# Optimization experiments

Measured on AMD Instinct MI355X. Metric: run time of the kernel, lower is better.

Reference implementation:

```python
import jax, jax.numpy as jnp
import numpy as np

B, N, DIM = 8, 16384, 256
DIM_HEAD, NUM_HEADS = 64, 8
D = DIM_HEAD * NUM_HEADS  # 512
SCALE = DIM_HEAD ** (-0.5)


def setup_inputs() -> dict:
    key = jax.random.key(0)
    ks = jax.random.split(key, 11)
    s = 0.02
    return {
        "x": jax.random.normal(ks[0], (B, N, DIM), dtype=jnp.float32),
        "Wq": jax.random.normal(ks[1], (DIM, D), dtype=jnp.float32) * s,
        "bq": jax.random.normal(ks[2], (D,), dtype=jnp.float32) * s,
        "Wk": jax.random.normal(ks[3], (DIM, D), dtype=jnp.float32) * s,
        "bk": jax.random.normal(ks[4], (D,), dtype=jnp.float32) * s,
        "qw": jax.random.normal(ks[5], (D, 1), dtype=jnp.float32),  # query_weight parameter
        "Wp": jax.random.normal(ks[6], (D, D), dtype=jnp.float32) * s,
        "bp": jax.random.normal(ks[7], (D,), dtype=jnp.float32) * s,
        "Wo": jax.random.normal(ks[8], (D, DIM_HEAD), dtype=jnp.float32) * s,
        "bo": jax.random.normal(ks[9], (DIM_HEAD,), dtype=jnp.float32) * s,
    }


def reference(x, Wq, bq, Wk, bk, qw, Wp, bp, Wo, bo):
    # query, key: [B, N, D]
    query = jnp.einsum("bnc,cd->bnd", x, Wq) + bq
    key = jnp.einsum("bnc,cd->bnd", x, Wk) + bk
    # per-token scalar score: [B, N, 1]
    score = (query @ qw) * SCALE
    # global attention context: sum over sequence axis -> [B, 1, D]
    attn_weight = jnp.sum(score * query, axis=1, keepdims=True)
    # broadcast (repeat over N), gate keys, project, residual add of query
    out = jnp.einsum("bnd,de->bne", attn_weight * key, Wp) + bp + query
    # output projection D -> dim_head: [B, N, DIM_HEAD]
    out = jnp.einsum("bnd,dh->bnh", out, Wo) + bo
    return out
```

## Files before the change

### kernel.cpp

```cpp
#include <hip/hip_runtime.h>
#include <hip/hip_bf16.h>


#define NN 16384
#define CC 256
#define DD 512
#define HH 64
#define SCALE_F 0.125f

#define OFF_SX    0
#define OFF_TSUM  2048
#define OFF_WQQ   2056
#define OFF_BQQ   2312
#define OFF_WPWO  2320
#define OFF_WQWO  35088
#define OFF_CBIAS 51472
#define OFF_BEFF  51536
#define OFF_WEFFT 52048

typedef unsigned short ushort_t;
typedef __attribute__((ext_vector_type(8))) short short8;
typedef __attribute__((ext_vector_type(4))) float floatx4;

__device__ __forceinline__ unsigned short f2bf(float f) {
    __hip_bfloat16 h = __float2bfloat16(f);
    return __builtin_bit_cast(unsigned short, h);
}

__global__ __launch_bounds__(256) void k_prep(
    const float* __restrict__ Wq, const float* __restrict__ bq,
    const float* __restrict__ qw, const float* __restrict__ Wp,
    const float* __restrict__ bp, const float* __restrict__ Wo,
    const float* __restrict__ bo, float* __restrict__ ws)
{
    __shared__ float lds[2056];
    const int tid = threadIdx.x;
    const int bid = blockIdx.x;

    if (bid < 128) {
        const int d0 = bid * 4;
        for (int i = tid; i < 2048; i += 256) lds[i] = Wp[d0 * 512 + i];
        __syncthreads();
        const int dl = tid >> 6, h = tid & 63;
        float acc = 0.f;
        for (int e = 0; e < 512; ++e)
            acc = fmaf(lds[dl * 512 + e], Wo[e * 64 + h], acc);
        ws[OFF_WPWO + (d0 + dl) * 64 + h] = acc;
    } else if (bid < 192) {
        const int c0 = (bid - 128) * 4;
        for (int i = tid; i < 2048; i += 256) lds[i] = Wq[c0 * 512 + i];
        __syncthreads();
        const int cl = tid >> 6, h = tid & 63;
        float acc = 0.f;
        for (int e = 0; e < 512; ++e)
            acc = fmaf(lds[cl * 512 + e], Wo[e * 64 + h], acc);
        ws[OFF_WQWO + (c0 + cl) * 64 + h] = acc;
    } else if (bid == 192) {
        float* lb = lds + 2048;
        for (int i = tid; i < 512; i += 256) lds[i] = qw[i];
        if (tid == 0) *lb = 0.f;
        __syncthreads();
        const float* wr = Wq + tid * 512;
        float acc = 0.f;
        for (int d = 0; d < 512; ++d) acc = fmaf(wr[d], lds[d], acc);
        ws[OFF_WQQ + tid] = acc;
        float pb = fmaf(bq[tid], lds[tid], bq[tid + 256] * lds[tid + 256]);
#pragma unroll
        for (int m = 1; m < 64; m <<= 1) pb += __shfl_xor(pb, m);
        if ((tid & 63) == 0) atomicAdd(lb, pb);
        __syncthreads();
        if (tid == 0) ws[OFF_BQQ] = *lb;
    } else if (bid == 193) {
        const int h = tid & 63, part = tid >> 6;
        float acc = 0.f;
        for (int d = part * 128; d < part * 128 + 128; ++d)
            acc = fmaf(bq[d] + bp[d], Wo[d * 64 + h], acc);
        lds[part * 64 + h] = acc;
        __syncthreads();
        if (tid < 64)
            ws[OFF_CBIAS + tid] = bo[tid] + lds[tid] + lds[64 + tid] +
                                  lds[128 + tid] + lds[192 + tid];
    } else {
        for (int i = tid; i < 2056; i += 256) ws[OFF_SX + i] = 0.f;
    }
}

__global__ __launch_bounds__(256) void k_phase1(
    const float* __restrict__ x, float* __restrict__ ws)
{
    const int tid  = threadIdx.x;
    const int lane = tid & 63;
    const int wave = tid >> 6;
    const int quad = lane >> 4;
    const int l15  = lane & 15;
    __shared__ float lacc[256];
    __shared__ float ltsum;

    floatx4 wv[4];
#pragma unroll
    for (int j = 0; j < 4; ++j)
        wv[j] = *(const floatx4*)(ws + OFF_WQQ + j * 64 + l15 * 4);
    const float bqq = ws[OFF_BQQ];

    const int vb = blockIdx.x;
    const int b = vb >> 7;
    const int rbase = (vb & 127) * 128;
    lacc[tid] = 0.f;
    if (tid == 0) ltsum = 0.f;
    __syncthreads();

    const float* xb = x + (size_t)b * NN * CC;
    const int r0 = rbase + wave * 32 + quad;
    floatx4 accs[4];
#pragma unroll
    for (int j = 0; j < 4; ++j)
#pragma unroll
        for (int k = 0; k < 4; ++k) accs[j][k] = 0.f;
    float ts = 0.f;

#pragma unroll 2
    for (int it = 0; it < 8; ++it) {
        const float* xr = xb + (size_t)(r0 + it * 4) * CC + l15 * 4;
        const floatx4 x0 = *(const floatx4*)(xr);
        const floatx4 x1 = *(const floatx4*)(xr + 64);
        const floatx4 x2 = *(const floatx4*)(xr + 128);
        const floatx4 x3 = *(const floatx4*)(xr + 192);
        float p = 0.f;
#pragma unroll
        for (int k = 0; k < 4; ++k) {
            p = fmaf(x0[k], wv[0][k], p);
            p = fmaf(x1[k], wv[1][k], p);
            p = fmaf(x2[k], wv[2][k], p);
            p = fmaf(x3[k], wv[3][k], p);
        }
        p += __shfl_xor(p, 1);
        p += __shfl_xor(p, 2);
        p += __shfl_xor(p, 4);
        p += __shfl_xor(p, 8);
        const float t = SCALE_F * (p + bqq);
        ts += t;
#pragma unroll
        for (int k = 0; k < 4; ++k) {
            accs[0][k] = fmaf(t, x0[k], accs[0][k]);
            accs[1][k] = fmaf(t, x1[k], accs[1][k]);
            accs[2][k] = fmaf(t, x2[k], accs[2][k]);
            accs[3][k] = fmaf(t, x3[k], accs[3][k]);
        }
    }

#pragma unroll
    for (int j = 0; j < 4; ++j)
#pragma unroll
        for (int k = 0; k < 4; ++k) {
            float v = accs[j][k];
            v += __shfl_xor(v, 16);
            v += __shfl_xor(v, 32);
            if (quad == 0) atomicAdd(&lacc[j * 64 + l15 * 4 + k], v);
        }
    if (l15 == 0) atomicAdd(&ltsum, ts);
    __syncthreads();
    atomicAdd(&ws[OFF_SX + b * 256 + tid], lacc[tid]);
    if (tid == 0) atomicAdd(&ws[OFF_TSUM + b], ltsum);
}

__global__ __launch_bounds__(256) void k_weff(
    const float* __restrict__ Wq, const float* __restrict__ bq,
    const float* __restrict__ Wk, const float* __restrict__ bk,
    float* __restrict__ ws)
{
    const int tid = threadIdx.x;
    const int b = blockIdx.y;
    const int c0 = blockIdx.x * 4;
    __shared__ float lsx[256];
    __shared__ float law[512];
    __shared__ float lred[256];
    __shared__ float lts;

    lsx[tid] = ws[OFF_SX + b * 256 + tid];
    if (tid == 0) lts = ws[OFF_TSUM + b];
    __syncthreads();
    const float tsum = lts;

    for (int d = tid; d < 512; d += 256) {
        float a0 = 0.f, a1 = 0.f, a2 = 0.f, a3 = 0.f;
        for (int c = 0; c < 256; c += 4) {
            a0 = fmaf(lsx[c + 0], Wq[(c + 0) * 512 + d], a0);
            a1 = fmaf(lsx[c + 1], Wq[(c + 1) * 512 + d], a1);
            a2 = fmaf(lsx[c + 2], Wq[(c + 2) * 512 + d], a2);
            a3 = fmaf(lsx[c + 3], Wq[(c + 3) * 512 + d], a3);
        }
        law[d] = tsum * bq[d] + ((a0 + a1) + (a2 + a3));
    }
    __syncthreads();

    const int cl = tid >> 6, h = tid & 63;
    const int c = c0 + cl;
    const float* wkr = Wk + (size_t)c * 512;
    const float* wp  = ws + OFF_WPWO;
    float a0 = 0.f, a1 = 0.f, a2 = 0.f, a3 = 0.f;
    for (int d = 0; d < 512; d += 4) {
        a0 = fmaf(wkr[d + 0] * law[d + 0], wp[(d + 0) * 64 + h], a0);
        a1 = fmaf(wkr[d + 1] * law[d + 1], wp[(d + 1) * 64 + h], a1);
        a2 = fmaf(wkr[d + 2] * law[d + 2], wp[(d + 2) * 64 + h], a2);
        a3 = fmaf(wkr[d + 3] * law[d + 3], wp[(d + 3) * 64 + h], a3);
    }
    const float acc = ws[OFF_WQWO + c * 64 + h] + ((a0 + a1) + (a2 + a3));

    ushort_t* wt = (ushort_t*)(ws + OFF_WEFFT) + (size_t)b * (HH * CC);
    wt[(size_t)h * CC + c] = f2bf(acc);

    if (blockIdx.x == 0) {
        const int part = tid >> 6;
        float a = 0.f;
        for (int d = part * 128; d < part * 128 + 128; ++d)
            a = fmaf(bk[d] * law[d], wp[d * 64 + h], a);
        lred[tid] = a;
        __syncthreads();
        if (tid < 64)
            ws[OFF_BEFF + b * 64 + tid] = ws[OFF_CBIAS + tid] + lred[tid] +
                lred[64 + tid] + lred[128 + tid] + lred[192 + tid];
    }
}

__global__ __launch_bounds__(256) void k_out(
    const float* __restrict__ x, const float* __restrict__ ws,
    float* __restrict__ out)
{
    const int tid  = threadIdx.x;
    const int lane = tid & 63;
    const int wave = tid >> 6;
    const int quad = lane >> 4;
    const int l15  = lane & 15;
    __shared__ __align__(16) ushort_t lwt[64 * 264];

    const int vb = blockIdx.x;
    const int b = vb >> 7;
    const int rt0 = vb & 127;
    const ushort_t* wt = (const ushort_t*)(ws + OFF_WEFFT) + (size_t)b * (HH * CC);
    for (int o = tid; o < 2048; o += 256) {
        const int h = o >> 5, seg = o & 31;
        *(short8*)(lwt + h * 264 + seg * 8) = *(const short8*)(wt + h * 256 + seg * 8);
    }
    __syncthreads();

    const float* beff = ws + OFF_BEFF + b * 64;
    float bias[4];
#pragma unroll
    for (int ht = 0; ht < 4; ++ht) bias[ht] = beff[ht * 16 + l15];

#pragma unroll
    for (int s = 0; s < 2; ++s) {
        const int row0 = (rt0 + s * 128) * 64 + wave * 16;
        const float* xr = x + ((size_t)b * NN + row0 + l15) * CC + quad * 8;
        short8 afrag[8];
#pragma unroll
        for (int kk = 0; kk < 8; ++kk) {
            const floatx4 u0 = *(const floatx4*)(xr + kk * 32);
            const floatx4 u1 = *(const floatx4*)(xr + kk * 32 + 4);
            short8 t;
            t[0] = (short)f2bf(u0[0]); t[1] = (short)f2bf(u0[1]);
            t[2] = (short)f2bf(u0[2]); t[3] = (short)f2bf(u0[3]);
            t[4] = (short)f2bf(u1[0]); t[5] = (short)f2bf(u1[1]);
            t[6] = (short)f2bf(u1[2]); t[7] = (short)f2bf(u1[3]);
            afrag[kk] = t;
        }
        floatx4 acc[4];
#pragma unroll
        for (int ht = 0; ht < 4; ++ht)
#pragma unroll
            for (int r = 0; r < 4; ++r) acc[ht][r] = 0.f;

#pragma unroll
        for (int kk = 0; kk < 8; ++kk)
#pragma unroll
            for (int ht = 0; ht < 4; ++ht) {
                const short8 bf =
                    *(const short8*)(lwt + (ht * 16 + l15) * 264 + quad * 8 + kk * 32);
                acc[ht] = __builtin_amdgcn_mfma_f32_16x16x32_bf16(
                    afrag[kk], bf, acc[ht], 0, 0, 0);
            }

#pragma unroll
        for (int ht = 0; ht < 4; ++ht) {
            const int h = ht * 16 + l15;
#pragma unroll
            for (int r = 0; r < 4; ++r) {
                const int row = row0 + quad * 4 + r;
                out[((size_t)b * NN + row) * HH + h] = acc[ht][r] + bias[ht];
            }
        }
    }
}

extern "C" void kernel_launch(void* const* d_in, const int* in_sizes, int n_in,
                              void* d_out, int out_size, void* d_ws, size_t ws_size,
                              hipStream_t stream) {
    const float* x  = (const float*)d_in[0];
    const float* Wq = (const float*)d_in[1];
    const float* bq = (const float*)d_in[2];
    const float* Wk = (const float*)d_in[3];
    const float* bk = (const float*)d_in[4];
    const float* qw = (const float*)d_in[5];
    const float* Wp = (const float*)d_in[6];
    const float* bp = (const float*)d_in[7];
    const float* Wo = (const float*)d_in[8];
    const float* bo = (const float*)d_in[9];
    float* ws  = (float*)d_ws;
    float* out = (float*)d_out;

    hipLaunchKernelGGL(k_prep,   dim3(195),    dim3(256), 0, stream,
                       Wq, bq, qw, Wp, bp, Wo, bo, ws);
    hipLaunchKernelGGL(k_phase1, dim3(1024),   dim3(256), 0, stream, x, ws);
    hipLaunchKernelGGL(k_weff,   dim3(64, 8),  dim3(256), 0, stream,
                       Wq, bq, Wk, bk, ws);
    hipLaunchKernelGGL(k_out,    dim3(1024),   dim3(256), 0, stream, x, ws, out);
}
```

Baseline: 308.2 us.

## Hoist attention-weight vector into its own kernel and prefetch x before LDS staging

The Wq·sx reduction that produces the per-batch attention weight vector is moved out of k_weff, where each of 64 blocks per batch recomputed it, into a new small k_aw kernel that writes it once to workspace. k_weff now reads it from global memory. Separately, k_out loads and converts its first x tile before staging the weight matrix into LDS, so the global loads overlap the LDS fill. This adds one kernel launch and a workspace round trip, and the prefetch raises register pressure.

Measured after the change: 301.3 us. 1.02x faster.

```diff
diff --git a/kernel.cpp b/kernel.cpp
--- a/kernel.cpp
+++ b/kernel.cpp
@@ -17,6 +17,7 @@
 #define OFF_CBIAS 51472
 #define OFF_BEFF  51536
 #define OFF_WEFFT 52048
+#define OFF_AW    117584
 
 typedef unsigned short ushort_t;
 typedef __attribute__((ext_vector_type(8))) short short8;
@@ -163,40 +164,47 @@
     if (tid == 0) atomicAdd(&ws[OFF_TSUM + b], ltsum);
 }
 
+__global__ __launch_bounds__(256) void k_aw(
+    const float* __restrict__ Wq, const float* __restrict__ bq,
+    float* __restrict__ ws)
+{
+    const int tid = threadIdx.x;
+    const int b = blockIdx.y;
+    const int d = blockIdx.x * 256 + tid;
+    __shared__ float lsx[256];
+    __shared__ float lts;
+    lsx[tid] = ws[OFF_SX + b * 256 + tid];
+    if (tid == 0) lts = ws[OFF_TSUM + b];
+    __syncthreads();
+
+    float a[8];
+#pragma unroll
+    for (int j = 0; j < 8; ++j) a[j] = 0.f;
+    for (int c = 0; c < 256; c += 8) {
+#pragma unroll
+        for (int j = 0; j < 8; ++j)
+            a[j] = fmaf(lsx[c + j], Wq[(c + j) * 512 + d], a[j]);
+    }
+    const float s = ((a[0] + a[1]) + (a[2] + a[3])) +
+                    ((a[4] + a[5]) + (a[6] + a[7]));
+    ws[OFF_AW + b * 512 + d] = lts * bq[d] + s;
+}
+
 __global__ __launch_bounds__(256) void k_weff(
-    const float* __restrict__ Wq, const float* __restrict__ bq,
     const float* __restrict__ Wk, const float* __restrict__ bk,
     float* __restrict__ ws)
 {
     const int tid = threadIdx.x;
     const int b = blockIdx.y;
     const int c0 = blockIdx.x * 4;
-    __shared__ float lsx[256];
-    __shared__ float law[512];
     __shared__ float lred[256];
-    __shared__ float lts;
-
-    lsx[tid] = ws[OFF_SX + b * 256 + tid];
-    if (tid == 0) lts = ws[OFF_TSUM + b];
-    __syncthreads();
-    const float tsum = lts;
-
-    for (int d = tid; d < 512; d += 256) {
-        float a0 = 0.f, a1 = 0.f, a2 = 0.f, a3 = 0.f;
-        for (int c = 0; c < 256; c += 4) {
-            a0 = fmaf(lsx[c + 0], Wq[(c + 0) * 512 + d], a0);
-            a1 = fmaf(lsx[c + 1], Wq[(c + 1) * 512 + d], a1);
-            a2 = fmaf(lsx[c + 2], Wq[(c + 2) * 512 + d], a2);
-            a3 = fmaf(lsx[c + 3], Wq[(c + 3) * 512 + d], a3);
-        }
-        law[d] = tsum * bq[d] + ((a0 + a1) + (a2 + a3));
-    }
-    __syncthreads();
 
     const int cl = tid >> 6, h = tid & 63;
     const int c = c0 + cl;
+    const float* law = ws + OFF_AW + (size_t)b * 512;
     const float* wkr = Wk + (size_t)c * 512;
     const float* wp  = ws + OFF_WPWO;
+
     float a0 = 0.f, a1 = 0.f, a2 = 0.f, a3 = 0.f;
     for (int d = 0; d < 512; d += 4) {
         a0 = fmaf(wkr[d + 0] * law[d + 0], wp[(d + 0) * 64 + h], a0);
@@ -236,6 +244,22 @@
     const int vb = blockIdx.x;
     const int b = vb >> 7;
     const int rt0 = vb & 127;
+
+    const int row0_0 = rt0 * 64 + wave * 16;
+    const float* xr0 = x + ((size_t)b * NN + row0_0 + l15) * CC + quad * 8;
+    short8 afrag0[8];
+#pragma unroll
+    for (int kk = 0; kk < 8; ++kk) {
+        const floatx4 u0 = *(const floatx4*)(xr0 + kk * 32);
+        const floatx4 u1 = *(const floatx4*)(xr0 + kk * 32 + 4);
+        short8 t;
+        t[0] = (short)f2bf(u0[0]); t[1] = (short)f2bf(u0[1]);
+        t[2] = (short)f2bf(u0[2]); t[3] = (short)f2bf(u0[3]);
+        t[4] = (short)f2bf(u1[0]); t[5] = (short)f2bf(u1[1]);
+        t[6] = (short)f2bf(u1[2]); t[7] = (short)f2bf(u1[3]);
+        afrag0[kk] = t;
+    }
+
     const ushort_t* wt = (const ushort_t*)(ws + OFF_WEFFT) + (size_t)b * (HH * CC);
     for (int o = tid; o < 2048; o += 256) {
         const int h = o >> 5, seg = o & 31;
@@ -248,28 +272,52 @@
 #pragma unroll
     for (int ht = 0; ht < 4; ++ht) bias[ht] = beff[ht * 16 + l15];
 
-#pragma unroll
-    for (int s = 0; s < 2; ++s) {
-        const int row0 = (rt0 + s * 128) * 64 + wave * 16;
-        const float* xr = x + ((size_t)b * NN + row0 + l15) * CC + quad * 8;
-        short8 afrag[8];
+    {
+        floatx4 acc[4];
+#pragma unroll
+        for (int ht = 0; ht < 4; ++ht)
+#pragma unroll
+            for (int r = 0; r < 4; ++r) acc[ht][r] = 0.f;
+#pragma unroll
+        for (int kk = 0; kk < 8; ++kk)
+#pragma unroll
+            for (int ht = 0; ht < 4; ++ht) {
+                const short8 bf =
+                    *(const short8*)(lwt + (ht * 16 + l15) * 264 + quad * 8 + kk * 32);
+                acc[ht] = __builtin_amdgcn_mfma_f32_16x16x32_bf16(
+                    afrag0[kk], bf, acc[ht], 0, 0, 0);
+            }
+#pragma unroll
+        for (int ht = 0; ht < 4; ++ht) {
+            const int h = ht * 16 + l15;
+#pragma unroll
+            for (int r = 0; r < 4; ++r) {
+                const int row = row0_0 + quad * 4 + r;
+                out[((size_t)b * NN + row) * HH + h] = acc[ht][r] + bias[ht];
+            }
+        }
+    }
+
+    {
+        const int row0_1 = (rt0 + 128) * 64 + wave * 16;
+        const float* xr1 = x + ((size_t)b * NN + row0_1 + l15) * CC + quad * 8;
+        short8 afrag1[8];
 #pragma unroll
         for (int kk = 0; kk < 8; ++kk) {
-            const floatx4 u0 = *(const floatx4*)(xr + kk * 32);
-            const floatx4 u1 = *(const floatx4*)(xr + kk * 32 + 4);
+            const floatx4 u0 = *(const floatx4*)(xr1 + kk * 32);
+            const floatx4 u1 = *(const floatx4*)(xr1 + kk * 32 + 4);
             short8 t;
             t[0] = (short)f2bf(u0[0]); t[1] = (short)f2bf(u0[1]);
             t[2] = (short)f2bf(u0[2]); t[3] = (short)f2bf(u0[3]);
             t[4] = (short)f2bf(u1[0]); t[5] = (short)f2bf(u1[1]);
             t[6] = (short)f2bf(u1[2]); t[7] = (short)f2bf(u1[3]);
-            afrag[kk] = t;
+            afrag1[kk] = t;
         }
         floatx4 acc[4];
 #pragma unroll
         for (int ht = 0; ht < 4; ++ht)
 #pragma unroll
             for (int r = 0; r < 4; ++r) acc[ht][r] = 0.f;
-
 #pragma unroll
         for (int kk = 0; kk < 8; ++kk)
 #pragma unroll
@@ -277,15 +325,14 @@
                 const short8 bf =
                     *(const short8*)(lwt + (ht * 16 + l15) * 264 + quad * 8 + kk * 32);
                 acc[ht] = __builtin_amdgcn_mfma_f32_16x16x32_bf16(
-                    afrag[kk], bf, acc[ht], 0, 0, 0);
+                    afrag1[kk], bf, acc[ht], 0, 0, 0);
             }
-
 #pragma unroll
         for (int ht = 0; ht < 4; ++ht) {
             const int h = ht * 16 + l15;
 #pragma unroll
             for (int r = 0; r < 4; ++r) {
-                const int row = row0 + quad * 4 + r;
+                const int row = row0_1 + quad * 4 + r;
                 out[((size_t)b * NN + row) * HH + h] = acc[ht][r] + bias[ht];
             }
         }
@@ -311,7 +358,7 @@
     hipLaunchKernelGGL(k_prep,   dim3(195),    dim3(256), 0, stream,
                        Wq, bq, qw, Wp, bp, Wo, bo, ws);
     hipLaunchKernelGGL(k_phase1, dim3(1024),   dim3(256), 0, stream, x, ws);
-    hipLaunchKernelGGL(k_weff,   dim3(64, 8),  dim3(256), 0, stream,
-                       Wq, bq, Wk, bk, ws);
+    hipLaunchKernelGGL(k_aw,     dim3(2, 8),   dim3(256), 0, stream, Wq, bq, ws);
+    hipLaunchKernelGGL(k_weff,   dim3(64, 8),  dim3(256), 0, stream, Wk, bk, ws);
     hipLaunchKernelGGL(k_out,    dim3(1024),   dim3(256), 0, stream, x, ws, out);
 }
```

## Split attention-weight matvec into its own kernel and reparallelize effective-weight build

Applied to the files above, without the earlier changes.

Adds a separate k_aw kernel that computes the per-batch attention-weight vector once and stores it in the workspace. Before, each of the 64 k_weff blocks per batch recomputed that full 256x512 matvec. k_weff now launches one block per input channel: 16 lane groups each own 4 outputs, the d dimension is split across 16 parts with float4 loads from the fused Wp·Wo matrix, and an LDS tree reduction combines the parts. Both new kernels are launched twice in a row; the second launches are redundant and only add launch and execution overhead.

After: 310.6 us. Within noise of the previous version (+0.8%).

```diff
diff --git a/kernel.cpp b/kernel.cpp
--- a/kernel.cpp
+++ b/kernel.cpp
@@ -17,6 +17,7 @@
 #define OFF_CBIAS 51472
 #define OFF_BEFF  51536
 #define OFF_WEFFT 52048
+#define OFF_AW    117584
 
 typedef unsigned short ushort_t;
 typedef __attribute__((ext_vector_type(8))) short short8;
@@ -163,62 +164,105 @@
     if (tid == 0) atomicAdd(&ws[OFF_TSUM + b], ltsum);
 }
 
+__global__ __launch_bounds__(256) void k_aw(
+    const float* __restrict__ Wq, const float* __restrict__ bq,
+    float* __restrict__ ws)
+{
+    const int tid = threadIdx.x;
+    const int b = blockIdx.y;
+    const int dl = tid & 63, part = tid >> 6;
+    const int d = blockIdx.x * 64 + dl;
+    __shared__ float lsx[256];
+    __shared__ float lred[256];
+    __shared__ float lts;
+    lsx[tid] = ws[OFF_SX + b * 256 + tid];
+    if (tid == 0) lts = ws[OFF_TSUM + b];
+    __syncthreads();
+
+    const int c0 = part * 64;
+    float a0 = 0.f, a1 = 0.f, a2 = 0.f, a3 = 0.f;
+    for (int c = c0; c < c0 + 64; c += 4) {
+        a0 = fmaf(lsx[c + 0], Wq[(c + 0) * 512 + d], a0);
+        a1 = fmaf(lsx[c + 1], Wq[(c + 1) * 512 + d], a1);
+        a2 = fmaf(lsx[c + 2], Wq[(c + 2) * 512 + d], a2);
+        a3 = fmaf(lsx[c + 3], Wq[(c + 3) * 512 + d], a3);
+    }
+    lred[tid] = ((a0 + a1) + (a2 + a3));
+    __syncthreads();
+    if (tid < 64) {
+        const float s = lred[tid] + lred[64 + tid] + lred[128 + tid] + lred[192 + tid];
+        const int dd = blockIdx.x * 64 + tid;
+        ws[OFF_AW + b * 512 + dd] = lts * bq[dd] + s;
+    }
+}
+
 __global__ __launch_bounds__(256) void k_weff(
-    const float* __restrict__ Wq, const float* __restrict__ bq,
     const float* __restrict__ Wk, const float* __restrict__ bk,
     float* __restrict__ ws)
 {
     const int tid = threadIdx.x;
     const int b = blockIdx.y;
-    const int c0 = blockIdx.x * 4;
-    __shared__ float lsx[256];
-    __shared__ float law[512];
-    __shared__ float lred[256];
-    __shared__ float lts;
-
-    lsx[tid] = ws[OFF_SX + b * 256 + tid];
-    if (tid == 0) lts = ws[OFF_TSUM + b];
-    __syncthreads();
-    const float tsum = lts;
-
-    for (int d = tid; d < 512; d += 256) {
-        float a0 = 0.f, a1 = 0.f, a2 = 0.f, a3 = 0.f;
-        for (int c = 0; c < 256; c += 4) {
-            a0 = fmaf(lsx[c + 0], Wq[(c + 0) * 512 + d], a0);
-            a1 = fmaf(lsx[c + 1], Wq[(c + 1) * 512 + d], a1);
-            a2 = fmaf(lsx[c + 2], Wq[(c + 2) * 512 + d], a2);
-            a3 = fmaf(lsx[c + 3], Wq[(c + 3) * 512 + d], a3);
-        }
-        law[d] = tsum * bq[d] + ((a0 + a1) + (a2 + a3));
-    }
-    __syncthreads();
-
-    const int cl = tid >> 6, h = tid & 63;
-    const int c = c0 + cl;
+    const int c = blockIdx.x;
+    const int hq = tid & 15;
+    const int part = tid >> 4;
+    __shared__ floatx4 lr[256];
+    __shared__ floatx4 lrb[256];
+
+    const float* law = ws + OFF_AW + (size_t)b * 512;
     const float* wkr = Wk + (size_t)c * 512;
-    const float* wp  = ws + OFF_WPWO;
-    float a0 = 0.f, a1 = 0.f, a2 = 0.f, a3 = 0.f;
-    for (int d = 0; d < 512; d += 4) {
-        a0 = fmaf(wkr[d + 0] * law[d + 0], wp[(d + 0) * 64 + h], a0);
-        a1 = fmaf(wkr[d + 1] * law[d + 1], wp[(d + 1) * 64 + h], a1);
-        a2 = fmaf(wkr[d + 2] * law[d + 2], wp[(d + 2) * 64 + h], a2);
-        a3 = fmaf(wkr[d + 3] * law[d + 3], wp[(d + 3) * 64 + h], a3);
-    }
-    const float acc = ws[OFF_WQWO + c * 64 + h] + ((a0 + a1) + (a2 + a3));
-
-    ushort_t* wt = (ushort_t*)(ws + OFF_WEFFT) + (size_t)b * (HH * CC);
-    wt[(size_t)h * CC + c] = f2bf(acc);
-
-    if (blockIdx.x == 0) {
-        const int part = tid >> 6;
-        float a = 0.f;
-        for (int d = part * 128; d < part * 128 + 128; ++d)
-            a = fmaf(bk[d] * law[d], wp[d * 64 + h], a);
-        lred[tid] = a;
-        __syncthreads();
-        if (tid < 64)
-            ws[OFF_BEFF + b * 64 + tid] = ws[OFF_CBIAS + tid] + lred[tid] +
-                lred[64 + tid] + lred[128 + tid] + lred[192 + tid];
+    const floatx4* wp4 = (const floatx4*)(ws + OFF_WPWO);
+    const bool do_beff = (c == 0);
+
+    floatx4 acc;
+    acc[0] = acc[1] = acc[2] = acc[3] = 0.f;
+    const int d0 = part * 32;
+    for (int d = d0; d < d0 + 32; ++d) {
+        const float g = wkr[d] * law[d];
+        const floatx4 w = wp4[d * 16 + hq];
+        acc[0] = fmaf(g, w[0], acc[0]);
+        acc[1] = fmaf(g, w[1], acc[1]);
+        acc[2] = fmaf(g, w[2], acc[2]);
+        acc[3] = fmaf(g, w[3], acc[3]);
+    }
+    lr[tid] = acc;
+
+    if (do_beff) {
+        floatx4 bacc;
+        bacc[0] = bacc[1] = bacc[2] = bacc[3] = 0.f;
+        for (int d = d0; d < d0 + 32; ++d) {
+            const float gb = bk[d] * law[d];
+            const floatx4 w = wp4[d * 16 + hq];
+            bacc[0] = fmaf(gb, w[0], bacc[0]);
+            bacc[1] = fmaf(gb, w[1], bacc[1]);
+            bacc[2] = fmaf(gb, w[2], bacc[2]);
+            bacc[3] = fmaf(gb, w[3], bacc[3]);
+        }
+        lrb[tid] = bacc;
+    }
+    __syncthreads();
+
+#pragma unroll
+    for (int s = 8; s >= 1; s >>= 1) {
+        if (part < s) {
+            lr[tid] += lr[tid + s * 16];
+            if (do_beff) lrb[tid] += lrb[tid + s * 16];
+        }
+        __syncthreads();
+    }
+
+    if (tid < 16) {
+        const floatx4 wq = *(const floatx4*)(ws + OFF_WQWO + c * 64 + tid * 4);
+        const floatx4 v = lr[tid];
+        ushort_t* wt = (ushort_t*)(ws + OFF_WEFFT) + (size_t)b * (HH * CC);
+        wt[(size_t)(tid * 4 + 0) * CC + c] = f2bf(wq[0] + v[0]);
+        wt[(size_t)(tid * 4 + 1) * CC + c] = f2bf(wq[1] + v[1]);
+        wt[(size_t)(tid * 4 + 2) * CC + c] = f2bf(wq[2] + v[2]);
+        wt[(size_t)(tid * 4 + 3) * CC + c] = f2bf(wq[3] + v[3]);
+        if (do_beff) {
+            const floatx4 cb = *(const floatx4*)(ws + OFF_CBIAS + tid * 4);
+            const floatx4 vb = lrb[tid];
+            *(floatx4*)(ws + OFF_BEFF + b * 64 + tid * 4) = cb + vb;
+        }
     }
 }
 
@@ -311,7 +355,9 @@
     hipLaunchKernelGGL(k_prep,   dim3(195),    dim3(256), 0, stream,
                        Wq, bq, qw, Wp, bp, Wo, bo, ws);
     hipLaunchKernelGGL(k_phase1, dim3(1024),   dim3(256), 0, stream, x, ws);
-    hipLaunchKernelGGL(k_weff,   dim3(64, 8),  dim3(256), 0, stream,
-                       Wq, bq, Wk, bk, ws);
+    hipLaunchKernelGGL(k_aw,     dim3(8, 8),   dim3(256), 0, stream, Wq, bq, ws);
+    hipLaunchKernelGGL(k_aw,     dim3(8, 8),   dim3(256), 0, stream, Wq, bq, ws);
+    hipLaunchKernelGGL(k_weff,   dim3(256, 8), dim3(256), 0, stream, Wk, bk, ws);
+    hipLaunchKernelGGL(k_weff,   dim3(256, 8), dim3(256), 0, stream, Wk, bk, ws);
     hipLaunchKernelGGL(k_out,    dim3(1024),   dim3(256), 0, stream, x, ws, out);
 }
```
